# Performance work log

Measured on AMD Instinct MI355X. Metric: run time of the kernel, lower is better.

## Reference

```python
import jax, jax.numpy as jnp
import numpy as np

CTX_RADIUS = 0.02
PRED_RADIUS = 0.05

def _knn_idx(xyz, k):
    # xyz: [N,3] -> [N,k] indices of k nearest neighbors (no self-loop)
    sq = jnp.sum(xyz * xyz, axis=-1)
    d2 = sq[:, None] + sq[None, :] - 2.0 * (xyz @ xyz.T)
    n = xyz.shape[0]
    d2 = d2 + jnp.eye(n, dtype=d2.dtype) * 1e10
    return jax.lax.top_k(-d2, k)[1]

def _edgeconv(xyz, feat, k, W1, b1, W2, b2):
    # PyG EdgeConv: message = mlp([x_i, x_j - x_i]), max-aggregate over neighbors
    x = jnp.concatenate([feat, xyz], axis=-1)          # [N, C+3]
    idx = _knn_idx(xyz, k)                             # [N, k]
    xj = x[idx]                                        # [N, k, C+3]
    xi = jnp.broadcast_to(x[:, None, :], xj.shape)
    msg = jnp.concatenate([xi, xj - xi], axis=-1)      # [N, k, 2*(C+3)]
    h = jax.nn.relu(msg @ W1 + b1) @ W2 + b2           # [N, k, C]
    return jnp.max(h, axis=1)                          # [N, C]

def _offset(feat, W1, b1, W2, b2):
    return jax.nn.relu(feat @ W1 + b1) @ W2 + b2

def _unit(v):
    return v / (jnp.linalg.norm(v, axis=-1, keepdims=True) + 1e-6)

def _forward(ctx_xyz, ctx_tokens, pred_tokens, noise_ctx, noise_pred,
             Wp, bp, We1, be1, We2, be2, Wc1, bc1, Wc2, bc2,
             Wq1, bq1, Wq2, bq2, Wf1, bf1, Wf2, bf2, k):
    B, P, _ = ctx_xyz.shape
    M = pred_tokens.shape[1]
    R_CTX = noise_ctx.shape[2]
    R_PRED = noise_pred.shape[2]
    C = Wp.shape[1]
    ec = lambda xyz, feat, kk: _edgeconv(xyz, feat, kk, We1, be1, We2, be2)

    # --- context branch ---
    ctx_feat = ctx_tokens @ Wp + bp                                  # [B,P,C]
    nc = _unit(noise_ctx) * CTX_RADIUS
    xyz_ctx = (ctx_xyz[:, :, None, :] + nc).reshape(B, P * R_CTX, 3)
    feat_ctx = jnp.broadcast_to(ctx_feat[:, :, None, :], (B, P, R_CTX, C)).reshape(B, P * R_CTX, C)
    feat_ctx = jax.vmap(lambda x, f: ec(x, f, k))(xyz_ctx, feat_ctx)
    xyz_ctx = xyz_ctx + _offset(feat_ctx, Wc1, bc1, Wc2, bc2)

    # --- prediction branch (batched over B*M tiny local graphs) ---
    anchor = jnp.mean(ctx_xyz, axis=1)                               # [B,3]
    pred_feat = pred_tokens @ Wp + bp                                # [B,M,C]
    npn = _unit(noise_pred) * PRED_RADIUS
    xyz_p = (anchor[:, None, None, :] + npn).reshape(B * M, R_PRED, 3)
    feat_p = jnp.broadcast_to(pred_feat[:, :, None, :], (B, M, R_PRED, C)).reshape(B * M, R_PRED, C)
    k_pred = min(k, R_PRED - 1)
    feat_p = jax.vmap(lambda x, f: ec(x, f, k_pred))(xyz_p, feat_p)
    xyz_p = xyz_p + _offset(feat_p, Wq1, bq1, Wq2, bq2)
    xyz_p = xyz_p.reshape(B, M * R_PRED, 3)
    feat_p = feat_p.reshape(B, M * R_PRED, C)

    # --- global refinement ---
    xyz_all = jnp.concatenate([xyz_ctx, xyz_p], axis=1)
    feat_all = jnp.concatenate([feat_ctx, feat_p], axis=1)
    feat_all = jax.vmap(lambda x, f: ec(x, f, k))(xyz_all, feat_all)
    xyz_all = xyz_all + _offset(feat_all, Wf1, bf1, Wf2, bf2)
    return xyz_all

def setup_inputs():
    key = jax.random.key(0)
    ks = jax.random.split(key, 20)
    B, P, M = 4, 384, 64
    C, TOK, R_CTX, R_PRED = 128, 1024, 12, 12
    w = lambda k_, s: jax.random.normal(k_, s, jnp.float32) * 0.02
    z = lambda s: jnp.zeros(s, jnp.float32)
    return {
        "ctx_xyz": jax.random.normal(ks[0], (B, P, 3), jnp.float32),
        "ctx_tokens": jax.random.normal(ks[1], (B, P, TOK), jnp.float32),
        "pred_tokens": jax.random.normal(ks[2], (B, M, TOK), jnp.float32),
        "noise_ctx": jax.random.normal(ks[3], (B, P, R_CTX, 3), jnp.float32),
        "noise_pred": jax.random.normal(ks[4], (B, M, R_PRED, 3), jnp.float32),
        "Wp": w(ks[5], (TOK, C)), "bp": z((C,)),
        "We1": w(ks[6], (2 * (C + 3), C)), "be1": z((C,)),
        "We2": w(ks[7], (C, C)), "be2": z((C,)),
        "Wc1": w(ks[8], (C, C)), "bc1": z((C,)),
        "Wc2": w(ks[9], (C, 3)), "bc2": z((3,)),
        "Wq1": w(ks[10], (C, C)), "bq1": z((C,)),
        "Wq2": w(ks[11], (C, 3)), "bq2": z((3,)),
        "Wf1": w(ks[12], (C, C)), "bf1": z((C,)),
        "Wf2": w(ks[13], (C, 3)), "bf2": z((3,)),
        "k": 8,
    }

def reference(ctx_xyz, ctx_tokens, pred_tokens, noise_ctx, noise_pred,
              Wp, bp, We1, be1, We2, be2, Wc1, bc1, Wc2, bc2,
              Wq1, bq1, Wq2, bq2, Wf1, bf1, Wf2, bf2, k):
    return _forward(ctx_xyz, ctx_tokens, pred_tokens, noise_ctx, noise_pred,
                    Wp, bp, We1, be1, We2, be2, Wc1, bc1, Wc2, bc2,
                    Wq1, bq1, Wq2, bq2, Wf1, bf1, Wf2, bf2, k)
```

## Files before the change

kernel.cpp:

```cpp
#include <hip/hip_runtime.h>
#include <math.h>

constexpr int B_   = 4;
constexpr int P_   = 384;
constexpr int M_   = 64;
constexpr int TOK  = 1024;
constexpr int C    = 128;
constexpr int RC   = 12;
constexpr int RP   = 12;
constexpr int KNN  = 8;
constexpr int GS   = 12;
constexpr int NCTX = P_ * RC;
constexpr int NPRD = M_ * RP;
constexpr int NALL = NCTX + NPRD;
constexpr int NG1  = NCTX / GS;
constexpr int NG3  = NALL / GS;
constexpr int TROWS = B_ * P_ + B_ * M_;
constexpr int KSPLIT = 4;

constexpr int AB1_BLOCKS   = (B_ * NCTX) / 8;
constexpr int KNN1_BLOCKS  = B_ * (NG1 / 4);
constexpr int AB2_BLOCKS   = (B_ * NPRD) / 8;
constexpr int KNS_BLOCKS   = (B_ * M_ * RP) / 256;
constexpr int P3G_BLOCKS   = (B_ * NALL) / 64;
constexpr int KNN3C_BLOCKS = B_ * (NG1 / 4);
constexpr int KNN3P_BLOCKS = (B_ * NPRD) / 4;

typedef __attribute__((ext_vector_type(8))) short bf16x8;
typedef __attribute__((ext_vector_type(4))) float f32x4;

__device__ inline unsigned short f32_to_bf16_rne(float x) {
  union { float f; unsigned int u; } v; v.f = x;
  unsigned int r = v.u + 0x7fffu + ((v.u >> 16) & 1u);
  return (unsigned short)(r >> 16);
}
__device__ inline float bf16_to_f32(unsigned short h) {
  union { float f; unsigned int u; } v; v.u = ((unsigned int)h) << 16;
  return v.f;
}
__device__ inline void split8(const f32x4& a0, const f32x4& a1, bf16x8& hi, bf16x8& lo) {
  float vals[8] = {a0.x, a0.y, a0.z, a0.w, a1.x, a1.y, a1.z, a1.w};
  union { unsigned short s[8]; bf16x8 v; } oh, ol;
  #pragma unroll
  for (int e = 0; e < 8; ++e) {
    unsigned short h = f32_to_bf16_rne(vals[e]);
    oh.s[e] = h;
    ol.s[e] = f32_to_bf16_rne(vals[e] - bf16_to_f32(h));
  }
  hi = oh.v; lo = ol.v;
}

__global__ __launch_bounds__(256) void prep1_kernel(const float* __restrict__ We1,
                                                    const float* __restrict__ We2,
                                                    const float* __restrict__ cxyz,
                                                    const float* __restrict__ Wc1,
                                                    const float* __restrict__ Wq1,
                                                    const float* __restrict__ Wf1,
                                                    float* __restrict__ Wcat,
                                                    unsigned short* __restrict__ we2hi,
                                                    unsigned short* __restrict__ we2lo,
                                                    float* __restrict__ anchor,
                                                    unsigned short* __restrict__ w1T_hi,
                                                    unsigned short* __restrict__ w1T_lo) {
  const int tid = threadIdx.x;
  if (blockIdx.x < 131) {
    int n = blockIdx.x * 256 + tid;
    int t = n >> 8, cc = n & 255;
    float v;
    if (cc < C) v = We1[t * C + cc] - We1[(131 + t) * C + cc];
    else        v = We1[(131 + t) * C + (cc - C)];
    Wcat[n] = v;
  } else if (blockIdx.x < 195) {
    int e = (blockIdx.x - 131) * 256 + tid;
    int n = e >> 7, k = e & 127;
    float w = We2[k * C + n];
    unsigned short h = f32_to_bf16_rne(w);
    we2hi[n * C + k] = h;
    we2lo[n * C + k] = f32_to_bf16_rne(w - bf16_to_f32(h));
  } else if (blockIdx.x == 195) {
    const int w = tid >> 6, lane = tid & 63;
    float ax = 0.f, ay = 0.f, az = 0.f;
    for (int p = lane; p < P_; p += 64) {
      const float* c = &cxyz[(w * P_ + p) * 3];
      ax += c[0]; ay += c[1]; az += c[2];
    }
    for (int o = 32; o > 0; o >>= 1) {
      ax += __shfl_down(ax, o);
      ay += __shfl_down(ay, o);
      az += __shfl_down(az, o);
    }
    if (lane == 0) {
      anchor[w * 3 + 0] = ax * (1.0f / (float)P_);
      anchor[w * 3 + 1] = ay * (1.0f / (float)P_);
      anchor[w * 3 + 2] = az * (1.0f / (float)P_);
    }
  } else {
    int e = (blockIdx.x - 196) * 256 + tid;
    int wsel = e >> 14, r = e & 16383;
    int c = r >> 7, k = r & 127;
    const float* W1s = (wsel == 0) ? Wc1 : (wsel == 1) ? Wq1 : Wf1;
    float w = W1s[k * C + c];
    unsigned short h = f32_to_bf16_rne(w);
    w1T_hi[(size_t)wsel * 16384 + c * 128 + k] = h;
    w1T_lo[(size_t)wsel * 16384 + c * 128 + k] = f32_to_bf16_rne(w - bf16_to_f32(h));
  }
}

__global__ __launch_bounds__(256) void prep2_kernel(const float* __restrict__ Wp,
                                                    const float* __restrict__ bp,
                                                    const float* __restrict__ Wcat,
                                                    const float* __restrict__ be1,
                                                    unsigned short* __restrict__ wbT_hi,
                                                    unsigned short* __restrict__ wbT_lo,
                                                    float* __restrict__ cb,
                                                    unsigned short* __restrict__ wcatT_hi,
                                                    unsigned short* __restrict__ wcatT_lo) {
  __shared__ float s_lds[4][128];
  const int tid = threadIdx.x;
  if (blockIdx.x < TOK / 4) {
    const int k0 = blockIdx.x * 4;
    for (int l = tid; l < 4 * 128; l += 256) {
      int r = l >> 7, f = l & 127;
      s_lds[r][f] = Wp[(k0 + r) * C + f];
    }
    __syncthreads();
    float acc[4] = {0.f, 0.f, 0.f, 0.f};
    #pragma unroll 4
    for (int f = 0; f < 128; ++f) {
      float wv = Wcat[f * 256 + tid];
      #pragma unroll
      for (int r = 0; r < 4; ++r) acc[r] = fmaf(s_lds[r][f], wv, acc[r]);
    }
    #pragma unroll
    for (int r = 0; r < 4; ++r) {
      unsigned short h = f32_to_bf16_rne(acc[r]);
      wbT_hi[(size_t)tid * TOK + k0 + r] = h;
      wbT_lo[(size_t)tid * TOK + k0 + r] = f32_to_bf16_rne(acc[r] - bf16_to_f32(h));
    }
  } else if (blockIdx.x == TOK / 4) {
    if (tid < 128) s_lds[0][tid] = bp[tid];
    __syncthreads();
    float a = (tid < 128) ? be1[tid] : 0.f;
    #pragma unroll 4
    for (int f = 0; f < 128; ++f) a = fmaf(s_lds[0][f], Wcat[f * 256 + tid], a);
    cb[tid] = a;
  } else {
    int e = (blockIdx.x - TOK / 4 - 1) * 256 + tid;
    int c = e >> 7, k = e & 127;
    float w = Wcat[k * 256 + c];
    unsigned short h = f32_to_bf16_rne(w);
    wcatT_hi[c * 128 + k] = h;
    wcatT_lo[c * 128 + k] = f32_to_bf16_rne(w - bf16_to_f32(h));
  }
}

__global__ __launch_bounds__(256) void build_all_kernel(const float* __restrict__ cxyz,
                                                        const float* __restrict__ noise_c,
                                                        const float* __restrict__ noise_p,
                                                        const float* __restrict__ anchor,
                                                        float* __restrict__ xyz_all,
                                                        int* __restrict__ radmax) {
  if (blockIdx.x < 72) {
    int n = blockIdx.x * 256 + threadIdx.x;
    if (n < B_ * NG3) radmax[n] = 0;
    int b = n / NCTX, i = n % NCTX, p = i / RC;
    float x = noise_c[n * 3 + 0], y = noise_c[n * 3 + 1], z = noise_c[n * 3 + 2];
    float s = 0.02f / (sqrtf(x * x + y * y + z * z) + 1e-6f);
    const float* c = &cxyz[(b * P_ + p) * 3];
    float* o = &xyz_all[(b * NALL + i) * 3];
    o[0] = c[0] + x * s;
    o[1] = c[1] + y * s;
    o[2] = c[2] + z * s;
  } else {
    int n = (blockIdx.x - 72) * 256 + threadIdx.x;
    int b = n / NPRD, i = n % NPRD;
    float x = noise_p[n * 3 + 0], y = noise_p[n * 3 + 1], z = noise_p[n * 3 + 2];
    float s = 0.05f / (sqrtf(x * x + y * y + z * z) + 1e-6f);
    const float* a = &anchor[b * 3];
    float* o = &xyz_all[(b * NALL + NCTX + i) * 3];
    o[0] = a[0] + x * s;
    o[1] = a[1] + y * s;
    o[2] = a[2] + z * s;
  }
}

__global__ __launch_bounds__(256) void t12_mfma_kernel(const float* __restrict__ ctx_tok,
                                                       const float* __restrict__ pred_tok,
                                                       const unsigned short* __restrict__ wbT_hi,
                                                       const unsigned short* __restrict__ wbT_lo,
                                                       float* __restrict__ Tpart) {
  __shared__ unsigned short ahi[64 * 128];
  __shared__ unsigned short alo[64 * 128];
  __shared__ unsigned short bhi[128 * 128];
  const int tid = threadIdx.x;
  const int r0 = blockIdx.x * 64;
  const int n0 = blockIdx.y * 128;
  const int s  = blockIdx.z;
  const float* src = (r0 < B_ * P_) ? (ctx_tok + (size_t)r0 * TOK)
                                    : (pred_tok + (size_t)(r0 - B_ * P_) * TOK);
  const int lane = tid & 63, w = tid >> 6;
  const int m = lane & 15, quad = lane >> 4;

  f32x4 acc[8];
  #pragma unroll
  for (int nt = 0; nt < 8; ++nt) acc[nt] = (f32x4){0.f, 0.f, 0.f, 0.f};

  #pragma unroll 1
  for (int kc = s * (8 / KSPLIT); kc < (s + 1) * (8 / KSPLIT); ++kc) {
    __syncthreads();
    #pragma unroll
    for (int i = 0; i < 4; ++i) {
      int task = tid + 256 * i;
      int r = task >> 4, c = task & 15;
      const float* sp = src + (size_t)r * TOK + kc * 128 + c * 8;
      f32x4 a0 = *(const f32x4*)sp;
      f32x4 a1 = *(const f32x4*)(sp + 4);
      bf16x8 oh, ol;
      split8(a0, a1, oh, ol);
      int dst = (r * 16 + (c ^ (r & 15))) * 8;
      *(bf16x8*)(ahi + dst) = oh;
      *(bf16x8*)(alo + dst) = ol;
    }
    #pragma unroll
    for (int i = 0; i < 8; ++i) {
      int task = tid + 256 * i;
      int n = task >> 4, c = task & 15;
      f32x4 v = *(const f32x4*)(wbT_hi + (size_t)(n0 + n) * TOK + kc * 128 + c * 8);
      *(f32x4*)(bhi + (n * 16 + (c ^ (n & 15))) * 8) = v;
    }
    __syncthreads();
    #pragma unroll
    for (int ks = 0; ks < 4; ++ks) {
      int c0 = ks * 4 + quad;
      int aoff = ((w * 16 + m) * 16 + (c0 ^ m)) * 8;
      bf16x8 av  = *(const bf16x8*)(ahi + aoff);
      bf16x8 av2 = *(const bf16x8*)(alo + aoff);
      #pragma unroll
      for (int nt = 0; nt < 8; ++nt) {
        int n = nt * 16 + m;
        bf16x8 bh = *(const bf16x8*)(bhi + (n * 16 + (c0 ^ m)) * 8);
        bf16x8 bl = *(const bf16x8*)(wbT_lo + (size_t)(n0 + n) * TOK + kc * 128 + c0 * 8);
        acc[nt] = __builtin_amdgcn_mfma_f32_16x16x32_bf16(av, bh, acc[nt], 0, 0, 0);
        acc[nt] = __builtin_amdgcn_mfma_f32_16x16x32_bf16(av, bl, acc[nt], 0, 0, 0);
        acc[nt] = __builtin_amdgcn_mfma_f32_16x16x32_bf16(av2, bh, acc[nt], 0, 0, 0);
      }
    }
  }
  #pragma unroll
  for (int nt = 0; nt < 8; ++nt) {
    int col = n0 + nt * 16 + m;
    #pragma unroll
    for (int reg = 0; reg < 4; ++reg) {
      int row = r0 + w * 16 + quad * 4 + reg;
      Tpart[((size_t)s * TROWS + row) * 256 + col] = acc[nt][reg];
    }
  }
}

template <int STAGE>
__device__ __forceinline__ void knn_wave_body(
    const float* __restrict__ xyz_all, const float* __restrict__ ctx_xyz,
    const float* __restrict__ anchor, const int* __restrict__ radmax,
    int b, int p, int lane,
    float4* own, int* gl, float4* tile, int* tilei,
    int* __restrict__ idx_out) {
  const int NG  = (STAGE == 1) ? NG1 : NG3;
  const int Npg = (STAGE == 1) ? NCTX : NALL;
  const float* base = xyz_all + (size_t)b * NALL * 3;
  const float* cxb  = ctx_xyz + (size_t)b * P_ * 3;
  const bool owner = lane < GS;
  const int qloc = p * GS + lane;

  auto sph = [&](int g) -> float4 {
    float4 c;
    float rad;
    if (STAGE == 1) {
      c = make_float4(cxb[g * 3 + 0], cxb[g * 3 + 1], cxb[g * 3 + 2], 0.f);
      rad = 0.0201f;
    } else {
      float moff = __int_as_float(radmax[b * NG3 + g]);
      if (g < NG1) {
        c = make_float4(cxb[g * 3 + 0], cxb[g * 3 + 1], cxb[g * 3 + 2], 0.f);
        rad = 0.0201f + moff * 1.0002f + 1e-6f;
      } else {
        c = make_float4(anchor[b * 3 + 0], anchor[b * 3 + 1], anchor[b * 3 + 2], 0.f);
        rad = 0.0501f + moff * 1.0002f + 1e-6f;
      }
    }
    c.w = rad;
    return c;
  };

  if (owner) {
    float x = base[qloc * 3 + 0], y = base[qloc * 3 + 1], z = base[qloc * 3 + 2];
    own[lane] = make_float4(x, y, z, x * x + y * y + z * z);
  }
  float qx = 0.f, qy = 0.f, qz = 0.f, sqi = 0.f;
  if (owner) {
    float4 q = own[lane];
    qx = q.x; qy = q.y; qz = q.z; sqi = q.w;
  }

  float bd[KNN];
  int   bi[KNN];
  #pragma unroll
  for (int u = 0; u < KNN; ++u) { bd[u] = 3e38f; bi[u] = 0x7fffffff; }

  #pragma unroll 1
  for (int j = 0; j < GS; ++j) {
    float4 cj = own[j];
    float d2 = sqi + cj.w - 2.0f * (qx * cj.x + qy * cj.y + qz * cj.z);
    if (owner && j != lane && d2 < bd[KNN - 1]) {
      bd[KNN - 1] = d2; bi[KNN - 1] = p * GS + j;
      #pragma unroll
      for (int u = KNN - 1; u > 0; --u) {
        if (bd[u] < bd[u - 1]) {
          float td = bd[u]; bd[u] = bd[u - 1]; bd[u - 1] = td;
          int   ti = bi[u]; bi[u] = bi[u - 1]; bi[u - 1] = ti;
        }
      }
    }
  }

  float t = owner ? bd[KNN - 1] : 0.f;
  #pragma unroll
  for (int mm = 1; mm < 64; mm <<= 1) t = fmaxf(t, __shfl_xor(t, mm));
  float r = sqrtf(fmaxf(t, 0.f)) * 1.001f + 1e-6f;

  const float4 gp = sph(p);
  const float rlim = r + gp.w;

  int ng = 0;
  #pragma unroll 1
  for (int gs0 = 0; gs0 < NG; gs0 += 64) {
    int g = gs0 + lane;
    bool ok = false;
    if (g < NG && g != p) {
      float4 gq = sph(g);
      float dx = gq.x - gp.x, dy = gq.y - gp.y, dz = gq.z - gp.z;
      float lim = rlim + gq.w;
      ok = (dx * dx + dy * dy + dz * dz) < lim * lim * 1.001f;
    }
    unsigned long long mask = __ballot(ok);
    if (ok) gl[ng + (int)__popcll(mask & ((1ull << lane) - 1ull))] = g;
    ng += (int)__popcll(mask);
  }

  const int total = ng * GS;
  #pragma unroll 1
  for (int cs = 0; cs < total; cs += 64) {
    int ci = cs + lane;
    if (ci < total) {
      int gg = gl[ci / GS];
      int j  = ci % GS;
      int jloc = gg * GS + j;
      float x = base[jloc * 3 + 0], y = base[jloc * 3 + 1], z = base[jloc * 3 + 2];
      tile[lane] = make_float4(x, y, z, x * x + y * y + z * z);
      tilei[lane] = jloc;
    }
    int nj = min(64, total - cs);
    #pragma unroll 1
    for (int jj = 0; jj < nj; ++jj) {
      float4 tt = tile[jj];
      int ti0 = tilei[jj];
      float d2 = sqi + tt.w - 2.0f * (qx * tt.x + qy * tt.y + qz * tt.z);
      if (owner && d2 < bd[KNN - 1]) {
        bd[KNN - 1] = d2; bi[KNN - 1] = ti0;
        #pragma unroll
        for (int u = KNN - 1; u > 0; --u) {
          if (bd[u] < bd[u - 1]) {
            float td = bd[u]; bd[u] = bd[u - 1]; bd[u - 1] = td;
            int   ti = bi[u]; bi[u] = bi[u - 1]; bi[u - 1] = ti;
          }
        }
      }
    }
  }

  if (owner) {
    int gid = b * Npg + qloc;
    #pragma unroll
    for (int u = 0; u < KNN; ++u) idx_out[gid * KNN + u] = b * Npg + bi[u];
  }
}

__device__ __forceinline__ void knn3_pred_wave(
    const float* __restrict__ xyz_all, const float* __restrict__ ctx_xyz,
    const float* __restrict__ anchor, const int* __restrict__ radmax,
    int b, int q, int lane, int* gl, int* __restrict__ idx_out) {
  const float* base = xyz_all + (size_t)b * NALL * 3;
  const float* cxb  = ctx_xyz + (size_t)b * P_ * 3;
  const int qloc = NCTX + q;
  const int p = NG1 + q / GS;

  const float qx = base[qloc * 3 + 0], qy = base[qloc * 3 + 1], qz = base[qloc * 3 + 2];
  const float sqi = qx * qx + qy * qy + qz * qz;

  float dcur = 3e38f;
  int   icur = 0x7fffffff;
  if (lane < GS) {
    int jloc = p * GS + lane;
    if (jloc != qloc) {
      float x = base[jloc * 3 + 0], y = base[jloc * 3 + 1], z = base[jloc * 3 + 2];
      dcur = sqi + (x * x + y * y + z * z) - 2.0f * (qx * x + qy * y + qz * z);
      icur = jloc;
    }
  }
  float t = 3e38f;
  #pragma unroll 1
  for (int r8 = 0; r8 < KNN; ++r8) {
    float d = dcur; int i = icur;
    #pragma unroll
    for (int mm = 1; mm < 64; mm <<= 1) {
      float od = __shfl_xor(d, mm);
      int   oi = __shfl_xor(i, mm);
      if (od < d || (od == d && oi < i)) { d = od; i = oi; }
    }
    t = d;
    if (icur == i) { dcur = 3e38f; icur = 0x7fffffff; }
  }
  float r = sqrtf(fmaxf(t, 0.f)) * 1.001f + 1e-6f;

  int ng = 0;
  #pragma unroll 1
  for (int gs0 = 0; gs0 < NG3; gs0 += 64) {
    int g = gs0 + lane;
    bool ok = false;
    if (g < NG3) {
      float cx, cy, cz, rad;
      float moff = __int_as_float(radmax[b * NG3 + g]) * 1.0002f + 1e-6f;
      if (g < NG1) {
        cx = cxb[g * 3 + 0]; cy = cxb[g * 3 + 1]; cz = cxb[g * 3 + 2];
        rad = 0.0201f + moff;
      } else {
        cx = anchor[b * 3 + 0]; cy = anchor[b * 3 + 1]; cz = anchor[b * 3 + 2];
        rad = 0.0501f + moff;
      }
      float dx = cx - qx, dy = cy - qy, dz = cz - qz;
      float lim = r + rad;
      ok = (dx * dx + dy * dy + dz * dz) < lim * lim * 1.001f;
    }
    unsigned long long mask = __ballot(ok);
    if (ok) gl[ng + (int)__popcll(mask & ((1ull << lane) - 1ull))] = g;
    ng += (int)__popcll(mask);
  }

  float bd[KNN];
  int   bi[KNN];
  #pragma unroll
  for (int u = 0; u < KNN; ++u) { bd[u] = 3e38f; bi[u] = 0x7fffffff; }
  const int total = ng * GS;
  #pragma unroll 2
  for (int ci = lane; ci < total; ci += 64) {
    int gg = gl[ci / GS];
    int j  = ci % GS;
    int jloc = gg * GS + j;
    float x = base[jloc * 3 + 0], y = base[jloc * 3 + 1], z = base[jloc * 3 + 2];
    float d2 = sqi + (x * x + y * y + z * z) - 2.0f * (qx * x + qy * y + qz * z);
    if (jloc != qloc && d2 < bd[KNN - 1]) {
      bd[KNN - 1] = d2; bi[KNN - 1] = jloc;
      #pragma unroll
      for (int u = KNN - 1; u > 0; --u) {
        if (bd[u] < bd[u - 1]) {
          float td = bd[u]; bd[u] = bd[u - 1]; bd[u - 1] = td;
          int   ti = bi[u]; bi[u] = bi[u - 1]; bi[u - 1] = ti;
        }
      }
    }
  }

  const int gid = b * NALL + qloc;
  #pragma unroll 1
  for (int r8 = 0; r8 < KNN; ++r8) {
    float d = bd[0]; int i = bi[0];
    #pragma unroll
    for (int mm = 1; mm < 64; mm <<= 1) {
      float od = __shfl_xor(d, mm);
      int   oi = __shfl_xor(i, mm);
      if (od < d || (od == d && oi < i)) { d = od; i = oi; }
    }
    if (lane == 0) idx_out[gid * KNN + r8] = b * NALL + i;
    if (bi[0] == i) {
      #pragma unroll
      for (int u = 0; u < KNN - 1; ++u) { bd[u] = bd[u + 1]; bi[u] = bi[u + 1]; }
      bd[KNN - 1] = 3e38f; bi[KNN - 1] = 0x7fffffff;
    }
  }
}

__global__ __launch_bounds__(256) void ab12_knn1_kernel(
    const float* __restrict__ Tp, const float* __restrict__ xyz_all,
    const float* __restrict__ Wcat, const float* __restrict__ cb,
    const float* __restrict__ ctx_xyz,
    float* __restrict__ AB, int* __restrict__ idx1) {
  __shared__ float4 own[4][GS];
  __shared__ int    gl[4][NG1];
  __shared__ float4 tile[4][64];
  __shared__ int    tilei[4][64];
  const int tid = threadIdx.x;
  if (blockIdx.x < AB1_BLOCKS) {
    const int base = blockIdx.x * 8;
    const float wx = Wcat[128 * 256 + tid];
    const float wy = Wcat[129 * 256 + tid];
    const float wz = Wcat[130 * 256 + tid];
    const float cbv = cb[tid];
    #pragma unroll
    for (int p = 0; p < 8; ++p) {
      int n = base + p;
      int b = n / NCTX, loc = n % NCTX;
      int trow = b * (NCTX / GS) + loc / GS;
      const float* xr = xyz_all + (size_t)(b * NALL + loc) * 3;
      float x = xr[0], y = xr[1], z = xr[2];
      float v = cbv;
      #pragma unroll
      for (int s = 0; s < KSPLIT; ++s)
        v += Tp[((size_t)s * TROWS + trow) * 256 + tid];
      v = fmaf(x, wx, v);
      v = fmaf(y, wy, v);
      v = fmaf(z, wz, v);
      AB[(size_t)n * 256 + tid] = v;
    }
  } else {
    int kblk = blockIdx.x - AB1_BLOCKS;
    int w = tid >> 6, lane = tid & 63;
    int b = kblk / (NG1 / 4);
    int p = (kblk % (NG1 / 4)) * 4 + w;
    knn_wave_body<1>(xyz_all, ctx_xyz, nullptr, nullptr, b, p, lane,
                     own[w], gl[w], tile[w], tilei[w], idx1);
  }
}

__global__ __launch_bounds__(256) void ab12_knn2_kernel(
    const float* __restrict__ Tp, const float* __restrict__ xyz_all,
    const float* __restrict__ Wcat, const float* __restrict__ cb,
    float* __restrict__ AB, int* __restrict__ idx2) {
  const int tid = threadIdx.x;
  if (blockIdx.x < AB2_BLOCKS) {
    const int base = blockIdx.x * 8;
    const float wx = Wcat[128 * 256 + tid];
    const float wy = Wcat[129 * 256 + tid];
    const float wz = Wcat[130 * 256 + tid];
    const float cbv = cb[tid];
    #pragma unroll
    for (int p = 0; p < 8; ++p) {
      int n = base + p;
      int b = n / NPRD, loc = n % NPRD;
      int trow = B_ * P_ + b * (NPRD / GS) + loc / GS;
      const float* xr = xyz_all + (size_t)(b * NALL + NCTX + loc) * 3;
      float x = xr[0], y = xr[1], z = xr[2];
      float v = cbv;
      #pragma unroll
      for (int s = 0; s < KSPLIT; ++s)
        v += Tp[((size_t)s * TROWS + trow) * 256 + tid];
      v = fmaf(x, wx, v);
      v = fmaf(y, wy, v);
      v = fmaf(z, wz, v);
      AB[(size_t)n * 256 + tid] = v;
    }
  } else {
    int q = (blockIdx.x - AB2_BLOCKS) * 256 + tid;
    int gr = q / RP, qi = q % RP;
    int b = gr / M_, w = gr % M_;
    const float* base = xyz_all + (size_t)(b * NALL + NCTX + w * RP) * 3;
    float cx[RP], cy[RP], cz[RP], cs[RP];
    #pragma unroll
    for (int j = 0; j < RP; ++j) {
      cx[j] = base[j * 3 + 0]; cy[j] = base[j * 3 + 1]; cz[j] = base[j * 3 + 2];
      cs[j] = cx[j] * cx[j] + cy[j] * cy[j] + cz[j] * cz[j];
    }
    float qx = cx[0], qy = cy[0], qz = cz[0], sqi = cs[0];
    #pragma unroll
    for (int j = 0; j < RP; ++j) {
      if (j == qi) { qx = cx[j]; qy = cy[j]; qz = cz[j]; sqi = cs[j]; }
    }
    float bd[KNN];
    int   bi[KNN];
    #pragma unroll
    for (int u = 0; u < KNN; ++u) { bd[u] = 3e38f; bi[u] = 0; }
    #pragma unroll
    for (int j = 0; j < RP; ++j) {
      float d2 = sqi + cs[j] - 2.0f * (qx * cx[j] + qy * cy[j] + qz * cz[j]);
      if (j != qi && d2 < bd[KNN - 1]) {
        bd[KNN - 1] = d2; bi[KNN - 1] = j;
        #pragma unroll
        for (int u = KNN - 1; u > 0; --u) {
          if (bd[u] < bd[u - 1]) {
            float td = bd[u]; bd[u] = bd[u - 1]; bd[u - 1] = td;
            int   ti = bi[u]; bi[u] = bi[u - 1]; bi[u - 1] = ti;
          }
        }
      }
    }
    #pragma unroll
    for (int u = 0; u < KNN; ++u) idx2[q * KNN + u] = gr * RP + bi[u];
  }
}

__global__ __launch_bounds__(256) void pre3_knn3_kernel(
    const float* __restrict__ feat, const float* __restrict__ xyz_all,
    const float* __restrict__ Wcat, const float* __restrict__ be1,
    const unsigned short* __restrict__ wcatT_hi, const unsigned short* __restrict__ wcatT_lo,
    const float* __restrict__ ctx_xyz, const float* __restrict__ anchor,
    const int* __restrict__ radmax,
    float* __restrict__ AB, int* __restrict__ idx3) {
  __shared__ float4 own[4][GS];
  __shared__ int    gl[4][NG3];
  __shared__ float4 tile[4][64];
  __shared__ int    tilei[4][64];
  const int tid = threadIdx.x;
  if (blockIdx.x < P3G_BLOCKS) {
    const int lane = tid & 63, w = tid >> 6;
    const int m = lane & 15, quad = lane >> 4;
    const int r0 = blockIdx.x * 64;
    const float* arow = feat + (size_t)(r0 + w * 16 + m) * C;

    f32x4 acc[16];
    #pragma unroll
    for (int nt = 0; nt < 16; ++nt) acc[nt] = (f32x4){0.f, 0.f, 0.f, 0.f};

    #pragma unroll
    for (int ks = 0; ks < 4; ++ks) {
      int k0 = ks * 32 + quad * 8;
      f32x4 a0 = *(const f32x4*)(arow + k0);
      f32x4 a1 = *(const f32x4*)(arow + k0 + 4);
      bf16x8 ahi, alo;
      split8(a0, a1, ahi, alo);
      #pragma unroll
      for (int nt = 0; nt < 16; ++nt) {
        int n = nt * 16 + m;
        bf16x8 bh = *(const bf16x8*)(wcatT_hi + n * 128 + k0);
        bf16x8 bl = *(const bf16x8*)(wcatT_lo + n * 128 + k0);
        acc[nt] = __builtin_amdgcn_mfma_f32_16x16x32_bf16(ahi, bh, acc[nt], 0, 0, 0);
        acc[nt] = __builtin_amdgcn_mfma_f32_16x16x32_bf16(ahi, bl, acc[nt], 0, 0, 0);
        acc[nt] = __builtin_amdgcn_mfma_f32_16x16x32_bf16(alo, bh, acc[nt], 0, 0, 0);
      }
    }
    float xr[4], yr[4], zr[4];
    #pragma unroll
    for (int reg = 0; reg < 4; ++reg) {
      int row = r0 + w * 16 + quad * 4 + reg;
      xr[reg] = xyz_all[row * 3 + 0];
      yr[reg] = xyz_all[row * 3 + 1];
      zr[reg] = xyz_all[row * 3 + 2];
    }
    #pragma unroll
    for (int nt = 0; nt < 16; ++nt) {
      int col = nt * 16 + m;
      float cbv = (col < C) ? be1[col] : 0.0f;
      float wx = Wcat[128 * 256 + col];
      float wy = Wcat[129 * 256 + col];
      float wz = Wcat[130 * 256 + col];
      #pragma unroll
      for (int reg = 0; reg < 4; ++reg) {
        int row = r0 + w * 16 + quad * 4 + reg;
        float v = acc[nt][reg] + cbv;
        v = fmaf(xr[reg], wx, v);
        v = fmaf(yr[reg], wy, v);
        v = fmaf(zr[reg], wz, v);
        AB[(size_t)row * 256 + col] = v;
      }
    }
  } else if (blockIdx.x < P3G_BLOCKS + KNN3C_BLOCKS) {
    int kblk = blockIdx.x - P3G_BLOCKS;
    int w = tid >> 6, lane = tid & 63;
    int b = kblk / (NG1 / 4);
    int p = (kblk % (NG1 / 4)) * 4 + w;
    knn_wave_body<3>(xyz_all, ctx_xyz, anchor, radmax, b, p, lane,
                     own[w], gl[w], tile[w], tilei[w], idx3);
  } else {
    int kblk = blockIdx.x - P3G_BLOCKS - KNN3C_BLOCKS;
    int w = tid >> 6, lane = tid & 63;
    int wid = kblk * 4 + w;
    int b = wid / NPRD, q = wid % NPRD;
    knn3_pred_wave(xyz_all, ctx_xyz, anchor, radmax, b, q, lane, gl[w], idx3);
  }
}

__global__ __launch_bounds__(256) void conv_mfma_kernel(const float* __restrict__ AB,
                                                        const int* __restrict__ idx,
                                                        const unsigned short* __restrict__ w2hi_g,
                                                        const unsigned short* __restrict__ w2lo_g,
                                                        const float* __restrict__ be2,
                                                        float* __restrict__ feat_out,
                                                        int NPB, int row_off) {
  __shared__ unsigned short hhi[64 * 128];
  __shared__ unsigned short hlo[64 * 128];
  __shared__ unsigned short w2hi[128 * 128];
  const int tid = threadIdx.x;
  const int base = blockIdx.x * 8;

  #pragma unroll
  for (int i = 0; i < 8; ++i) {
    int q = tid + 256 * i;
    int n = q >> 4, c = q & 15;
    f32x4 v = *(const f32x4*)(w2hi_g + n * 128 + c * 8);
    *(f32x4*)(w2hi + (n * 16 + (c ^ (n & 15))) * 8) = v;
  }

  #pragma unroll
  for (int i = 0; i < 4; ++i) {
    int task = tid + 256 * i;
    int r = task >> 4, c = task & 15;
    int p = r >> 3, nb = r & 7;
    int g = base + p;
    int j = idx[g * KNN + nb];
    const float* aP = AB + (size_t)g * 256 + c * 8;
    const float* bP = AB + (size_t)j * 256 + 128 + c * 8;
    f32x4 a0 = *(const f32x4*)aP;
    f32x4 a1 = *(const f32x4*)(aP + 4);
    f32x4 b0 = *(const f32x4*)bP;
    f32x4 b1 = *(const f32x4*)(bP + 4);
    f32x4 s0 = {fmaxf(a0.x + b0.x, 0.f), fmaxf(a0.y + b0.y, 0.f),
                fmaxf(a0.z + b0.z, 0.f), fmaxf(a0.w + b0.w, 0.f)};
    f32x4 s1 = {fmaxf(a1.x + b1.x, 0.f), fmaxf(a1.y + b1.y, 0.f),
                fmaxf(a1.z + b1.z, 0.f), fmaxf(a1.w + b1.w, 0.f)};
    bf16x8 oh, ol;
    split8(s0, s1, oh, ol);
    int dst = (r * 16 + (c ^ (r & 15))) * 8;
    *(bf16x8*)(hhi + dst) = oh;
    *(bf16x8*)(hlo + dst) = ol;
  }
  __syncthreads();

  const int lane = tid & 63, w = tid >> 6;
  const int m = lane & 15, quad = lane >> 4;
  f32x4 acc[8];
  #pragma unroll
  for (int nt = 0; nt < 8; ++nt) acc[nt] = (f32x4){0.f, 0.f, 0.f, 0.f};

  #pragma unroll 1
  for (int ks = 0; ks < 4; ++ks) {
    int c0 = ks * 4 + quad;
    int rowA = w * 16 + m;
    int aoff = (rowA * 16 + (c0 ^ m)) * 8;
    bf16x8 ahi = *(const bf16x8*)(hhi + aoff);
    bf16x8 alo = *(const bf16x8*)(hlo + aoff);
    #pragma unroll
    for (int nt = 0; nt < 8; ++nt) {
      int n = nt * 16 + m;
      bf16x8 bhi = *(const bf16x8*)(w2hi + (n * 16 + (c0 ^ m)) * 8);
      bf16x8 blo = *(const bf16x8*)(w2lo_g + n * 128 + c0 * 8);
      acc[nt] = __builtin_amdgcn_mfma_f32_16x16x32_bf16(ahi, bhi, acc[nt], 0, 0, 0);
      acc[nt] = __builtin_amdgcn_mfma_f32_16x16x32_bf16(ahi, blo, acc[nt], 0, 0, 0);
      acc[nt] = __builtin_amdgcn_mfma_f32_16x16x32_bf16(alo, bhi, acc[nt], 0, 0, 0);
    }
  }

  int pt = 2 * w + (quad >> 1);
  int g = base + pt;
  int b = g / NPB, loc = g % NPB;
  float* orow = feat_out + (size_t)(b * NALL + row_off + loc) * C;
  bool writer = (quad & 1) == 0;
  #pragma unroll
  for (int nt = 0; nt < 8; ++nt) {
    float v = fmaxf(fmaxf(acc[nt].x, acc[nt].y), fmaxf(acc[nt].z, acc[nt].w));
    v = fmaxf(v, __shfl_xor(v, 16));
    if (writer) {
      int col = nt * 16 + m;
      orow[col] = v + be2[col];
    }
  }
}

__global__ __launch_bounds__(256) void offset_mfma_kernel(
    const float* __restrict__ feat,
    const unsigned short* __restrict__ w1T_hi, const unsigned short* __restrict__ w1T_lo,
    const float* __restrict__ b1, const float* __restrict__ W2, const float* __restrict__ b2,
    const float* __restrict__ xyz_in, float* __restrict__ xyz_out,
    int NPB, int row_off, int* __restrict__ radmax) {
  const int tid = threadIdx.x;
  const int lane = tid & 63, w = tid >> 6;
  const int m = lane & 15, quad = lane >> 4;
  const int r0 = blockIdx.x * 64;

  int nA = r0 + w * 16 + m;
  int bA = nA / NPB, locA = nA % NPB;
  const float* arow = feat + (size_t)(bA * NALL + row_off + locA) * C;

  f32x4 acc[8];
  #pragma unroll
  for (int nt = 0; nt < 8; ++nt) acc[nt] = (f32x4){0.f, 0.f, 0.f, 0.f};

  #pragma unroll
  for (int ks = 0; ks < 4; ++ks) {
    int k0 = ks * 32 + quad * 8;
    f32x4 a0 = *(const f32x4*)(arow + k0);
    f32x4 a1 = *(const f32x4*)(arow + k0 + 4);
    bf16x8 ahi, alo;
    split8(a0, a1, ahi, alo);
    #pragma unroll
    for (int nt = 0; nt < 8; ++nt) {
      int n = nt * 16 + m;
      bf16x8 bh = *(const bf16x8*)(w1T_hi + n * 128 + k0);
      bf16x8 bl = *(const bf16x8*)(w1T_lo + n * 128 + k0);
      acc[nt] = __builtin_amdgcn_mfma_f32_16x16x32_bf16(ahi, bh, acc[nt], 0, 0, 0);
      acc[nt] = __builtin_amdgcn_mfma_f32_16x16x32_bf16(ahi, bl, acc[nt], 0, 0, 0);
      acc[nt] = __builtin_amdgcn_mfma_f32_16x16x32_bf16(alo, bh, acc[nt], 0, 0, 0);
    }
  }

  float p0[4] = {0.f, 0.f, 0.f, 0.f};
  float p1[4] = {0.f, 0.f, 0.f, 0.f};
  float p2[4] = {0.f, 0.f, 0.f, 0.f};
  #pragma unroll
  for (int nt = 0; nt < 8; ++nt) {
    int col = nt * 16 + m;
    float b1v = b1[col];
    float w20 = W2[col * 3 + 0], w21 = W2[col * 3 + 1], w22 = W2[col * 3 + 2];
    #pragma unroll
    for (int reg = 0; reg < 4; ++reg) {
      float h = fmaxf(acc[nt][reg] + b1v, 0.0f);
      p0[reg] = fmaf(h, w20, p0[reg]);
      p1[reg] = fmaf(h, w21, p1[reg]);
      p2[reg] = fmaf(h, w22, p2[reg]);
    }
  }
  #pragma unroll
  for (int o = 1; o < 16; o <<= 1) {
    #pragma unroll
    for (int reg = 0; reg < 4; ++reg) {
      p0[reg] += __shfl_xor(p0[reg], o);
      p1[reg] += __shfl_xor(p1[reg], o);
      p2[reg] += __shfl_xor(p2[reg], o);
    }
  }
  if (m == 0) {
    float b20 = b2[0], b21 = b2[1], b22 = b2[2];
    #pragma unroll
    for (int reg = 0; reg < 4; ++reg) {
      int nO = r0 + w * 16 + quad * 4 + reg;
      int b = nO / NPB, loc = nO % NPB;
      int row = (b * NALL + row_off + loc) * 3;
      float o0 = p0[reg] + b20;
      float o1 = p1[reg] + b21;
      float o2 = p2[reg] + b22;
      xyz_out[row + 0] = xyz_in[row + 0] + o0;
      xyz_out[row + 1] = xyz_in[row + 1] + o1;
      xyz_out[row + 2] = xyz_in[row + 2] + o2;
      if (radmax != nullptr) {
        float mag = sqrtf(o0 * o0 + o1 * o1 + o2 * o2);
        atomicMax(radmax + b * NG3 + (row_off + loc) / GS, __float_as_int(mag));
      }
    }
  }
}

extern "C" void kernel_launch(void* const* d_in, const int* in_sizes, int n_in,
                              void* d_out, int out_size, void* d_ws, size_t ws_size,
                              hipStream_t stream) {
  (void)in_sizes; (void)n_in; (void)out_size; (void)ws_size;
  const float* ctx_xyz   = (const float*)d_in[0];
  const float* ctx_tok   = (const float*)d_in[1];
  const float* pred_tok  = (const float*)d_in[2];
  const float* noise_ctx = (const float*)d_in[3];
  const float* noise_prd = (const float*)d_in[4];
  const float* Wp  = (const float*)d_in[5];
  const float* bp  = (const float*)d_in[6];
  const float* We1 = (const float*)d_in[7];
  const float* be1 = (const float*)d_in[8];
  const float* We2 = (const float*)d_in[9];
  const float* be2 = (const float*)d_in[10];
  const float* Wc1 = (const float*)d_in[11];
  const float* bc1 = (const float*)d_in[12];
  const float* Wc2 = (const float*)d_in[13];
  const float* bc2 = (const float*)d_in[14];
  const float* Wq1 = (const float*)d_in[15];
  const float* bq1 = (const float*)d_in[16];
  const float* Wq2 = (const float*)d_in[17];
  const float* bq2 = (const float*)d_in[18];
  const float* Wf1 = (const float*)d_in[19];
  const float* bf1 = (const float*)d_in[20];
  const float* Wf2 = (const float*)d_in[21];
  const float* bf2 = (const float*)d_in[22];
  float* out = (float*)d_out;

  float* ws        = (float*)d_ws;
  float* T         = ws;
  float* anchor    = T + TROWS * 256;
  float* xyz_all   = anchor + 16;
  float* feat_in   = xyz_all + B_ * NALL * 3;
  float* feat_out  = feat_in + B_ * NALL * C;
  float* AB        = feat_out + B_ * NALL * C;
  float* Wcat      = AB + B_ * NALL * 256;
  float* cb        = Wcat + 131 * 256;
  int*   idx1      = (int*)(cb + 256);
  int*   idx2      = idx1 + B_ * NCTX * KNN;
  int*   idx3      = idx2 + B_ * NPRD * KNN;
  unsigned short* we2hi = (unsigned short*)(idx3 + B_ * NALL * KNN);
  unsigned short* we2lo = we2hi + C * C;
  int*   radmax    = (int*)(we2lo + C * C);
  unsigned short* wcatT_hi = (unsigned short*)(radmax + B_ * NG3);
  unsigned short* wcatT_lo = wcatT_hi + 256 * 128;
  unsigned short* w1T_hi   = wcatT_lo + 256 * 128;
  unsigned short* w1T_lo   = w1T_hi + 3 * C * C;
  unsigned short* wbT_hi = (unsigned short*)AB;
  unsigned short* wbT_lo = wbT_hi + 256 * TOK;
  float* Tpart = feat_out;

  prep1_kernel<<<388, 256, 0, stream>>>(We1, We2, ctx_xyz, Wc1, Wq1, Wf1,
                                        Wcat, we2hi, we2lo, anchor, w1T_hi, w1T_lo);
  prep2_kernel<<<TOK / 4 + 1 + 128, 256, 0, stream>>>(Wp, bp, Wcat, be1,
                                                      wbT_hi, wbT_lo, cb,
                                                      wcatT_hi, wcatT_lo);
  build_all_kernel<<<72 + 12, 256, 0, stream>>>(ctx_xyz, noise_ctx, noise_prd, anchor,
                                                xyz_all, radmax);

  t12_mfma_kernel<<<dim3(TROWS / 64, 2, KSPLIT), 256, 0, stream>>>(ctx_tok, pred_tok,
                                                                   wbT_hi, wbT_lo, Tpart);

  ab12_knn1_kernel<<<AB1_BLOCKS + KNN1_BLOCKS, 256, 0, stream>>>(Tpart, xyz_all, Wcat, cb,
                                                                 ctx_xyz, AB, idx1);
  conv_mfma_kernel<<<(B_ * NCTX) / 8, 256, 0, stream>>>(AB, idx1, we2hi, we2lo, be2, feat_in, NCTX, 0);
  offset_mfma_kernel<<<(B_ * NCTX) / 64, 256, 0, stream>>>(feat_in, w1T_hi, w1T_lo,
                                                           bc1, Wc2, bc2,
                                                           xyz_all, xyz_all, NCTX, 0, radmax);

  ab12_knn2_kernel<<<AB2_BLOCKS + KNS_BLOCKS, 256, 0, stream>>>(Tpart, xyz_all, Wcat, cb, AB, idx2);
  conv_mfma_kernel<<<(B_ * NPRD) / 8, 256, 0, stream>>>(AB, idx2, we2hi, we2lo, be2, feat_in, NPRD, NCTX);
  offset_mfma_kernel<<<(B_ * NPRD) / 64, 256, 0, stream>>>(feat_in, w1T_hi + C * C, w1T_lo + C * C,
                                                           bq1, Wq2, bq2,
                                                           xyz_all, xyz_all, NPRD, NCTX, radmax);

  pre3_knn3_kernel<<<P3G_BLOCKS + KNN3C_BLOCKS + KNN3P_BLOCKS, 256, 0, stream>>>(
      feat_in, xyz_all, Wcat, be1, wcatT_hi, wcatT_lo, ctx_xyz, anchor, radmax, AB, idx3);
  conv_mfma_kernel<<<(B_ * NALL) / 8, 256, 0, stream>>>(AB, idx3, we2hi, we2lo, be2, feat_out, NALL, 0);
  offset_mfma_kernel<<<(B_ * NALL) / 64, 256, 0, stream>>>(feat_out, w1T_hi + 2 * C * C, w1T_lo + 2 * C * C,
                                                           bf1, Wf2, bf2,
                                                           xyz_all, out, NALL, 0, nullptr);
}
```

Baseline: 398.5 us.

## Merge context and prediction stages into single AB/KNN, conv and offset launches

Fuses the stage-1 context and stage-2 prediction pipelines, which are independent, into one AB-building plus KNN kernel, one conv kernel and one offset kernel over all points. Neighbor indices now use global NALL-based row numbering, so the conv and offset kernels drop their per-branch remapping arguments. The offset kernel picks context or prediction weights per block. This removes three kernel launches and their serialization, and lets the two branches share the GPU at once. The cost is a few extra per-block branches.

```diff
diff --git a/kernel.cpp b/kernel.cpp
--- a/kernel.cpp
+++ b/kernel.cpp
@@ -18,9 +18,8 @@
 constexpr int TROWS = B_ * P_ + B_ * M_;
 constexpr int KSPLIT = 4;
 
-constexpr int AB1_BLOCKS   = (B_ * NCTX) / 8;
+constexpr int ABALL_BLOCKS = (B_ * NALL) / 8;
 constexpr int KNN1_BLOCKS  = B_ * (NG1 / 4);
-constexpr int AB2_BLOCKS   = (B_ * NPRD) / 8;
 constexpr int KNS_BLOCKS   = (B_ * M_ * RP) / 256;
 constexpr int P3G_BLOCKS   = (B_ * NALL) / 64;
 constexpr int KNN3C_BLOCKS = B_ * (NG1 / 4);
@@ -265,7 +264,6 @@
     float4* own, int* gl, float4* tile, int* tilei,
     int* __restrict__ idx_out) {
   const int NG  = (STAGE == 1) ? NG1 : NG3;
-  const int Npg = (STAGE == 1) ? NCTX : NALL;
   const float* base = xyz_all + (size_t)b * NALL * 3;
   const float* cxb  = ctx_xyz + (size_t)b * P_ * 3;
   const bool owner = lane < GS;
@@ -378,9 +376,9 @@
   }
 
   if (owner) {
-    int gid = b * Npg + qloc;
-    #pragma unroll
-    for (int u = 0; u < KNN; ++u) idx_out[gid * KNN + u] = b * Npg + bi[u];
+    int gid = b * NALL + qloc;
+    #pragma unroll
+    for (int u = 0; u < KNN; ++u) idx_out[gid * KNN + u] = b * NALL + bi[u];
   }
 }
 
@@ -488,17 +486,17 @@
   }
 }
 
-__global__ __launch_bounds__(256) void ab12_knn1_kernel(
+__global__ __launch_bounds__(256) void ab12_knn12_kernel(
     const float* __restrict__ Tp, const float* __restrict__ xyz_all,
     const float* __restrict__ Wcat, const float* __restrict__ cb,
     const float* __restrict__ ctx_xyz,
-    float* __restrict__ AB, int* __restrict__ idx1) {
+    float* __restrict__ AB, int* __restrict__ idxA) {
   __shared__ float4 own[4][GS];
   __shared__ int    gl[4][NG1];
   __shared__ float4 tile[4][64];
   __shared__ int    tilei[4][64];
   const int tid = threadIdx.x;
-  if (blockIdx.x < AB1_BLOCKS) {
+  if (blockIdx.x < ABALL_BLOCKS) {
     const int base = blockIdx.x * 8;
     const float wx = Wcat[128 * 256 + tid];
     const float wy = Wcat[129 * 256 + tid];
@@ -507,9 +505,10 @@
     #pragma unroll
     for (int p = 0; p < 8; ++p) {
       int n = base + p;
-      int b = n / NCTX, loc = n % NCTX;
-      int trow = b * (NCTX / GS) + loc / GS;
-      const float* xr = xyz_all + (size_t)(b * NALL + loc) * 3;
+      int b = n / NALL, row = n % NALL;
+      int trow = (row < NCTX) ? (b * (NCTX / GS) + row / GS)
+                              : (B_ * P_ + b * (NPRD / GS) + (row - NCTX) / GS);
+      const float* xr = xyz_all + (size_t)n * 3;
       float x = xr[0], y = xr[1], z = xr[2];
       float v = cbv;
       #pragma unroll
@@ -520,45 +519,15 @@
       v = fmaf(z, wz, v);
       AB[(size_t)n * 256 + tid] = v;
     }
-  } else {
-    int kblk = blockIdx.x - AB1_BLOCKS;
+  } else if (blockIdx.x < ABALL_BLOCKS + KNN1_BLOCKS) {
+    int kblk = blockIdx.x - ABALL_BLOCKS;
     int w = tid >> 6, lane = tid & 63;
     int b = kblk / (NG1 / 4);
     int p = (kblk % (NG1 / 4)) * 4 + w;
     knn_wave_body<1>(xyz_all, ctx_xyz, nullptr, nullptr, b, p, lane,
-                     own[w], gl[w], tile[w], tilei[w], idx1);
-  }
-}
-
-__global__ __launch_bounds__(256) void ab12_knn2_kernel(
-    const float* __restrict__ Tp, const float* __restrict__ xyz_all,
-    const float* __restrict__ Wcat, const float* __restrict__ cb,
-    float* __restrict__ AB, int* __restrict__ idx2) {
-  const int tid = threadIdx.x;
-  if (blockIdx.x < AB2_BLOCKS) {
-    const int base = blockIdx.x * 8;
-    const float wx = Wcat[128 * 256 + tid];
-    const float wy = Wcat[129 * 256 + tid];
-    const float wz = Wcat[130 * 256 + tid];
-    const float cbv = cb[tid];
-    #pragma unroll
-    for (int p = 0; p < 8; ++p) {
-      int n = base + p;
-      int b = n / NPRD, loc = n % NPRD;
-      int trow = B_ * P_ + b * (NPRD / GS) + loc / GS;
-      const float* xr = xyz_all + (size_t)(b * NALL + NCTX + loc) * 3;
-      float x = xr[0], y = xr[1], z = xr[2];
-      float v = cbv;
-      #pragma unroll
-      for (int s = 0; s < KSPLIT; ++s)
-        v += Tp[((size_t)s * TROWS + trow) * 256 + tid];
-      v = fmaf(x, wx, v);
-      v = fmaf(y, wy, v);
-      v = fmaf(z, wz, v);
-      AB[(size_t)n * 256 + tid] = v;
-    }
+                     own[w], gl[w], tile[w], tilei[w], idxA);
   } else {
-    int q = (blockIdx.x - AB2_BLOCKS) * 256 + tid;
+    int q = (blockIdx.x - ABALL_BLOCKS - KNN1_BLOCKS) * 256 + tid;
     int gr = q / RP, qi = q % RP;
     int b = gr / M_, w = gr % M_;
     const float* base = xyz_all + (size_t)(b * NALL + NCTX + w * RP) * 3;
@@ -591,8 +560,10 @@
         }
       }
     }
-    #pragma unroll
-    for (int u = 0; u < KNN; ++u) idx2[q * KNN + u] = gr * RP + bi[u];
+    int gid = b * NALL + NCTX + w * RP + qi;
+    #pragma unroll
+    for (int u = 0; u < KNN; ++u)
+      idxA[gid * KNN + u] = b * NALL + NCTX + w * RP + bi[u];
   }
 }
 
@@ -681,8 +652,7 @@
                                                         const unsigned short* __restrict__ w2hi_g,
                                                         const unsigned short* __restrict__ w2lo_g,
                                                         const float* __restrict__ be2,
-                                                        float* __restrict__ feat_out,
-                                                        int NPB, int row_off) {
+                                                        float* __restrict__ feat_out) {
   __shared__ unsigned short hhi[64 * 128];
   __shared__ unsigned short hlo[64 * 128];
   __shared__ unsigned short w2hi[128 * 128];
@@ -731,6 +701,7 @@
   #pragma unroll 1
   for (int ks = 0; ks < 4; ++ks) {
     int c0 = ks * 4 + quad;
+    int k0 = c0 * 8;
     int rowA = w * 16 + m;
     int aoff = (rowA * 16 + (c0 ^ m)) * 8;
     bf16x8 ahi = *(const bf16x8*)(hhi + aoff);
@@ -739,7 +710,7 @@
     for (int nt = 0; nt < 8; ++nt) {
       int n = nt * 16 + m;
       bf16x8 bhi = *(const bf16x8*)(w2hi + (n * 16 + (c0 ^ m)) * 8);
-      bf16x8 blo = *(const bf16x8*)(w2lo_g + n * 128 + c0 * 8);
+      bf16x8 blo = *(const bf16x8*)(w2lo_g + n * 128 + k0);
       acc[nt] = __builtin_amdgcn_mfma_f32_16x16x32_bf16(ahi, bhi, acc[nt], 0, 0, 0);
       acc[nt] = __builtin_amdgcn_mfma_f32_16x16x32_bf16(ahi, blo, acc[nt], 0, 0, 0);
       acc[nt] = __builtin_amdgcn_mfma_f32_16x16x32_bf16(alo, bhi, acc[nt], 0, 0, 0);
@@ -748,8 +719,7 @@
 
   int pt = 2 * w + (quad >> 1);
   int g = base + pt;
-  int b = g / NPB, loc = g % NPB;
-  float* orow = feat_out + (size_t)(b * NALL + row_off + loc) * C;
+  float* orow = feat_out + (size_t)g * C;
   bool writer = (quad & 1) == 0;
   #pragma unroll
   for (int nt = 0; nt < 8; ++nt) {
@@ -764,18 +734,25 @@
 
 __global__ __launch_bounds__(256) void offset_mfma_kernel(
     const float* __restrict__ feat,
-    const unsigned short* __restrict__ w1T_hi, const unsigned short* __restrict__ w1T_lo,
-    const float* __restrict__ b1, const float* __restrict__ W2, const float* __restrict__ b2,
+    const unsigned short* __restrict__ w1T_hi_c, const unsigned short* __restrict__ w1T_lo_c,
+    const float* __restrict__ b1_c, const float* __restrict__ W2_c, const float* __restrict__ b2_c,
+    const unsigned short* __restrict__ w1T_hi_p, const unsigned short* __restrict__ w1T_lo_p,
+    const float* __restrict__ b1_p, const float* __restrict__ W2_p, const float* __restrict__ b2_p,
     const float* __restrict__ xyz_in, float* __restrict__ xyz_out,
-    int NPB, int row_off, int* __restrict__ radmax) {
+    int* __restrict__ radmax) {
   const int tid = threadIdx.x;
   const int lane = tid & 63, w = tid >> 6;
   const int m = lane & 15, quad = lane >> 4;
   const int r0 = blockIdx.x * 64;
-
-  int nA = r0 + w * 16 + m;
-  int bA = nA / NPB, locA = nA % NPB;
-  const float* arow = feat + (size_t)(bA * NALL + row_off + locA) * C;
+  const bool isCtx = (r0 % NALL) < NCTX;
+
+  const unsigned short* w1T_hi = isCtx ? w1T_hi_c : w1T_hi_p;
+  const unsigned short* w1T_lo = isCtx ? w1T_lo_c : w1T_lo_p;
+  const float* b1 = isCtx ? b1_c : b1_p;
+  const float* W2 = isCtx ? W2_c : W2_p;
+  const float* b2 = isCtx ? b2_c : b2_p;
+
+  const float* arow = feat + (size_t)(r0 + w * 16 + m) * C;
 
   f32x4 acc[8];
   #pragma unroll
@@ -829,8 +806,7 @@
     #pragma unroll
     for (int reg = 0; reg < 4; ++reg) {
       int nO = r0 + w * 16 + quad * 4 + reg;
-      int b = nO / NPB, loc = nO % NPB;
-      int row = (b * NALL + row_off + loc) * 3;
+      int row = nO * 3;
       float o0 = p0[reg] + b20;
       float o1 = p1[reg] + b21;
       float o2 = p2[reg] + b22;
@@ -838,8 +814,9 @@
       xyz_out[row + 1] = xyz_in[row + 1] + o1;
       xyz_out[row + 2] = xyz_in[row + 2] + o2;
       if (radmax != nullptr) {
+        int b = nO / NALL, loc = nO % NALL;
         float mag = sqrtf(o0 * o0 + o1 * o1 + o2 * o2);
-        atomicMax(radmax + b * NG3 + (row_off + loc) / GS, __float_as_int(mag));
+        atomicMax(radmax + b * NG3 + loc / GS, __float_as_int(mag));
       }
     }
   }
@@ -883,9 +860,8 @@
   float* AB        = feat_out + B_ * NALL * C;
   float* Wcat      = AB + B_ * NALL * 256;
   float* cb        = Wcat + 131 * 256;
-  int*   idx1      = (int*)(cb + 256);
-  int*   idx2      = idx1 + B_ * NCTX * KNN;
-  int*   idx3      = idx2 + B_ * NPRD * KNN;
+  int*   idxA      = (int*)(cb + 256);
+  int*   idx3      = idxA + B_ * NALL * KNN;
   unsigned short* we2hi = (unsigned short*)(idx3 + B_ * NALL * KNN);
   unsigned short* we2lo = we2hi + C * C;
   int*   radmax    = (int*)(we2lo + C * C);
@@ -908,23 +884,21 @@
   t12_mfma_kernel<<<dim3(TROWS / 64, 2, KSPLIT), 256, 0, stream>>>(ctx_tok, pred_tok,
                                                                    wbT_hi, wbT_lo, Tpart);
 
-  ab12_knn1_kernel<<<AB1_BLOCKS + KNN1_BLOCKS, 256, 0, stream>>>(Tpart, xyz_all, Wcat, cb,
-                                                                 ctx_xyz, AB, idx1);
-  conv_mfma_kernel<<<(B_ * NCTX) / 8, 256, 0, stream>>>(AB, idx1, we2hi, we2lo, be2, feat_in, NCTX, 0);
-  offset_mfma_kernel<<<(B_ * NCTX) / 64, 256, 0, stream>>>(feat_in, w1T_hi, w1T_lo,
-                                                           bc1, Wc2, bc2,
-                                                           xyz_all, xyz_all, NCTX, 0, radmax);
-
-  ab12_knn2_kernel<<<AB2_BLOCKS + KNS_BLOCKS, 256, 0, stream>>>(Tpart, xyz_all, Wcat, cb, AB, idx2);
-  conv_mfma_kernel<<<(B_ * NPRD) / 8, 256, 0, stream>>>(AB, idx2, we2hi, we2lo, be2, feat_in, NPRD, NCTX);
-  offset_mfma_kernel<<<(B_ * NPRD) / 64, 256, 0, stream>>>(feat_in, w1T_hi + C * C, w1T_lo + C * C,
-                                                           bq1, Wq2, bq2,
-                                                           xyz_all, xyz_all, NPRD, NCTX, radmax);
+  ab12_knn12_kernel<<<ABALL_BLOCKS + KNN1_BLOCKS + KNS_BLOCKS, 256, 0, stream>>>(
+      Tpart, xyz_all, Wcat, cb, ctx_xyz, AB, idxA);
+  conv_mfma_kernel<<<ABALL_BLOCKS, 256, 0, stream>>>(AB, idxA, we2hi, we2lo, be2, feat_in);
+  offset_mfma_kernel<<<(B_ * NALL) / 64, 256, 0, stream>>>(
+      feat_in,
+      w1T_hi, w1T_lo, bc1, Wc2, bc2,
+      w1T_hi + C * C, w1T_lo + C * C, bq1, Wq2, bq2,
+      xyz_all, xyz_all, radmax);
 
   pre3_knn3_kernel<<<P3G_BLOCKS + KNN3C_BLOCKS + KNN3P_BLOCKS, 256, 0, stream>>>(
       feat_in, xyz_all, Wcat, be1, wcatT_hi, wcatT_lo, ctx_xyz, anchor, radmax, AB, idx3);
-  conv_mfma_kernel<<<(B_ * NALL) / 8, 256, 0, stream>>>(AB, idx3, we2hi, we2lo, be2, feat_out, NALL, 0);
-  offset_mfma_kernel<<<(B_ * NALL) / 64, 256, 0, stream>>>(feat_out, w1T_hi + 2 * C * C, w1T_lo + 2 * C * C,
-                                                           bf1, Wf2, bf2,
-                                                           xyz_all, out, NALL, 0, nullptr);
-}
+  conv_mfma_kernel<<<ABALL_BLOCKS, 256, 0, stream>>>(AB, idx3, we2hi, we2lo, be2, feat_out);
+  offset_mfma_kernel<<<(B_ * NALL) / 64, 256, 0, stream>>>(
+      feat_out,
+      w1T_hi + 2 * C * C, w1T_lo + 2 * C * C, bf1, Wf2, bf2,
+      w1T_hi + 2 * C * C, w1T_lo + 2 * C * C, bf1, Wf2, bf2,
+      xyz_all, out, nullptr);
+}
```

Measured after the change: 375.6 us. -5.7%, faster.
